# Kernel optimization log

Hardware: AMD Instinct MI355X
Metric: run time of the kernel (lower is better)

The kernel has to match this reference:

```python
import jax, jax.numpy as jnp
import numpy as np

NUM_K = 10
T = 1.0  # softmax temperature (forward default)


def setup_inputs() -> dict:
    key = jax.random.key(0)
    k1, k2, k3, k4 = jax.random.split(key, 4)
    B, H, P, D = 64, 12, 197, 64
    return {
        "att_s": jax.random.normal(k1, (B, H, P, P), dtype=jnp.float32),
        "att_t": jax.random.normal(k2, (B, H, P, P), dtype=jnp.float32),
        "v_s": jax.random.normal(k3, (B, H, P, D), dtype=jnp.float32),
        "v_t": jax.random.normal(k4, (B, H, P, D), dtype=jnp.float32),
    }


def _topk_masked_attend(att, v):
    # att: [B,H,P,P] logits, v: [B,H,P,D]
    a = jax.nn.softmax(att / T, axis=-1)
    # kth-largest value per row acts as the threshold (torch.topk semantics)
    margin = jax.lax.top_k(a, NUM_K)[0][..., -1]           # [B,H,P]
    a = a * (a >= margin[..., None])                        # keep top-k entries
    norm = a.sum(-1)                                        # [B,H,P]
    return jnp.einsum("bhpq,bhqd->bhpd", a, v) / norm[..., None]


def reference(att_s, att_t, v_s, v_t):
    out_s = _topk_masked_attend(att_s, v_s)
    out_t = _topk_masked_attend(att_t, v_t)
    # nn.MSELoss default reduction='mean'
    return jnp.mean(jnp.square(out_s - out_t))
```

## Files before the change

### kernel.cpp

```cpp
#include <hip/hip_runtime.h>
#include <cstdint>
#include <cfloat>

#define NK 10
constexpr int Pp   = 197;
constexpr int Dd   = 64;
constexpr int ROWS = 64 * 12 * 197;
constexpr int BLK  = 256;
constexpr int RPB  = 256;
constexpr int NBLK = ROWS / RPB;
constexpr int CH   = 32;
constexpr int NFULL = Pp / CH;
constexpr int TAIL  = Pp - NFULL * CH;
constexpr float INV_N = 1.0f / 9682944.0f;

constexpr int RPB_B = 16;
constexpr int NB_B  = ROWS / RPB_B;

__device__ __forceinline__ uint32_t fbits(float x) { return __float_as_uint(x); }
__device__ __forceinline__ float    bfl(uint32_t u) { return __uint_as_float(u); }

template <int CW>
__device__ __forceinline__ void consume_chunk(const float* __restrict__ trow,
                                              float a[NK]) {
#pragma unroll
  for (int j = 0; j < CW; ++j) {
    float x = trow[j];
#pragma unroll
    for (int s = 0; s < NK - 1; ++s) a[s] = fmaxf(a[s], fminf(x, a[s + 1]));
    a[NK - 1] = fmaxf(a[NK - 1], x);
  }
}

__device__ __forceinline__ void load_chunk_regs(const float* __restrict__ slab,
                                                int c, int t, float pf[CH]) {
  if (c < NFULL) {
    const int r0 = t >> 5, j = t & 31;
    const uint32_t col = (uint32_t)(c * CH + j);
    const float* p = slab + c * CH + r0 * Pp + j;
#pragma unroll
    for (int i = 0; i < CH; ++i) {
      float x = __builtin_nontemporal_load(&p[i * 8 * Pp]);
      pf[i] = bfl((fbits(x) & 0xFFFFFF00u) | col);
    }
  } else {
    const float* cbase = slab + NFULL * CH;
#pragma unroll
    for (int i = 0; i < TAIL; ++i) {
      int e = t + i * BLK;
      int r = e / TAIL, j = e % TAIL;
      float x = __builtin_nontemporal_load(&cbase[r * Pp + j]);
      pf[i] = bfl((fbits(x) & 0xFFFFFF00u) | (uint32_t)(NFULL * CH + j));
    }
  }
}

__device__ __forceinline__ void store_chunk(float (*tile)[CH + 1], int c, int t,
                                            const float pf[CH]) {
  if (c < NFULL) {
    const int r0 = t >> 5, j = t & 31;
#pragma unroll
    for (int i = 0; i < CH; ++i) tile[r0 + 8 * i][j] = pf[i];
  } else {
#pragma unroll
    for (int i = 0; i < TAIL; ++i) {
      int e = t + i * BLK;
      tile[e / TAIL][e % TAIL] = pf[i];
    }
  }
}

__global__ __launch_bounds__(BLK, 4) void select_kernel(
    const float* __restrict__ att_s, const float* __restrict__ att_t,
    float* __restrict__ wpk ) {
  __shared__ float tile[RPB][CH + 1];

  const int t = threadIdx.x;
  const int bi = blockIdx.x;
  const int tensor = (bi >= NBLK) ? 1 : 0;
  const int slab = bi - tensor * NBLK;
  const float* A = tensor ? att_t : att_s;
  const int blockRow0 = slab * RPB;

  float a[NK];
#pragma unroll
  for (int k = 0; k < NK; ++k) a[k] = -FLT_MAX;

  const float* slabp = A + (size_t)blockRow0 * Pp;
  float pf[CH];

  load_chunk_regs(slabp, 0, t, pf);
  for (int c = 0; c <= NFULL; ++c) {
    __syncthreads();
    store_chunk(tile, c, t, pf);
    __syncthreads();
    if (c < NFULL) {
      load_chunk_regs(slabp, c + 1, t, pf);
      consume_chunk<CH>(tile[t], a);
    } else {
      consume_chunk<TAIL>(tile[t], a);
    }
  }

  float mx = a[NK - 1];
  float e[NK], s = 0.f;
#pragma unroll
  for (int k = 0; k < NK; ++k) { e[k] = __expf(a[k] - mx); s += e[k]; }
  float inv = 1.0f / s;

  __syncthreads();
  float* flat = &tile[0][0];
#pragma unroll
  for (int k = 0; k < NK; ++k) {
    float w = e[k] * inv;
    flat[t * NK + k] = bfl((fbits(w) & 0xFFFFFF00u) | (fbits(a[k]) & 0xFFu));
  }
  __syncthreads();
  float* dst = wpk + ((size_t)tensor * ROWS + blockRow0) * NK;
#pragma unroll
  for (int i = 0; i < NK; ++i) dst[t + i * BLK] = flat[t + i * BLK];
}

__global__ __launch_bounds__(1024) void gather_kernel(
    const float* __restrict__ v_s, const float* __restrict__ v_t,
    const float* __restrict__ wpk, float* __restrict__ partial) {
  const int t = threadIdx.x, wv = t >> 6, l = t & 63;
  int row = blockIdx.x * RPB_B + wv;
  row = __builtin_amdgcn_readfirstlane(row);
  const int bh = row / Pp;
  const float* vsb = v_s + (size_t)bh * (Pp * Dd) + l;
  const float* vtb = v_t + (size_t)bh * (Pp * Dd) + l;
  const float* w0 = wpk + (size_t)row * NK;
  const float* w1 = wpk + ((size_t)ROWS + row) * NK;

  float acc = 0.f;
#pragma unroll
  for (int k = 0; k < NK; ++k) {
    float w = w0[k];
    int idx = (int)(fbits(w) & 0xFFu);
    acc = fmaf(w, vsb[idx * Dd], acc);
  }
#pragma unroll
  for (int k = 0; k < NK; ++k) {
    float w = w1[k];
    int idx = (int)(fbits(w) & 0xFFu);
    acc = fmaf(-w, vtb[idx * Dd], acc);
  }
  float sq = acc * acc;
#pragma unroll
  for (int off = 32; off > 0; off >>= 1) sq += __shfl_xor(sq, off, 64);

  __shared__ float red[RPB_B];
  if (l == 0) red[wv] = sq;
  __syncthreads();
  if (t == 0) {
    float tot = 0.f;
#pragma unroll
    for (int i = 0; i < RPB_B; ++i) tot += red[i];
    partial[blockIdx.x] = tot;
  }
}

__global__ __launch_bounds__(1024) void reduce_kernel(
    const float* __restrict__ partial, float* __restrict__ out) {
  const int t = threadIdx.x, wv = t >> 6, l = t & 63;
  float s = 0.f;
  for (int i = t; i < NB_B; i += 1024) s += partial[i];
#pragma unroll
  for (int off = 32; off > 0; off >>= 1) s += __shfl_xor(s, off, 64);
  __shared__ float red[16];
  if (l == 0) red[wv] = s;
  __syncthreads();
  if (t == 0) {
    float tot = 0.f;
#pragma unroll
    for (int i = 0; i < 16; ++i) tot += red[i];
    out[0] = tot * INV_N;
  }
}

extern "C" void kernel_launch(void* const* d_in, const int* in_sizes, int n_in,
                              void* d_out, int out_size, void* d_ws,
                              size_t ws_size, hipStream_t stream) {
  const float* att_s = (const float*)d_in[0];
  const float* att_t = (const float*)d_in[1];
  const float* v_s = (const float*)d_in[2];
  const float* v_t = (const float*)d_in[3];
  float* out = (float*)d_out;

  float* wpk = (float*)d_ws;
  float* partial = wpk + (size_t)2 * ROWS * NK;

  select_kernel<<<2 * NBLK, BLK, 0, stream>>>(att_s, att_t, wpk);
  gather_kernel<<<NB_B, 1024, 0, stream>>>(v_s, v_t, wpk, partial);
  reduce_kernel<<<1, 1024, 0, stream>>>(partial, out);
}
```

Before: 379.0 us.

## Split each row's top-k across two threads with pairwise insertion and vector loads

The select kernel now assigns two threads per row, each keeping a top-10 over half the columns, and merges them with a bitonic-style max of one list against the other's reversed top half via lane shuffles. Global loads become 16-byte vector loads, the tile stride is padded for vector LDS access, and elements are inserted two at a time with a pair-insert network. Rows per block drop to 128 and the occupancy hint rises to 8, aiming for more parallelism and fewer instructions per element in this compute-bound selection step. The merge keeps only the top 5 of the elementwise maxes, which is valid for a bitonic merge, and unaligned f4 loads depend on the declared 4-byte alignment.

```diff
diff --git a/kernel.cpp b/kernel.cpp
--- a/kernel.cpp
+++ b/kernel.cpp
@@ -7,118 +7,152 @@
 constexpr int Dd   = 64;
 constexpr int ROWS = 64 * 12 * 197;
 constexpr int BLK  = 256;
-constexpr int RPB  = 256;
-constexpr int NBLK = ROWS / RPB;
+constexpr int RPB  = 128;
+constexpr int NSLAB = ROWS / RPB;
 constexpr int CH   = 32;
-constexpr int NFULL = Pp / CH;
-constexpr int TAIL  = Pp - NFULL * CH;
+constexpr int NCH  = Pp / CH;
+constexpr int TAILC = Pp - NCH * CH;
+constexpr int LDW  = CH + 4;
 constexpr float INV_N = 1.0f / 9682944.0f;
 
 constexpr int RPB_B = 16;
 constexpr int NB_B  = ROWS / RPB_B;
 
+typedef float f4 __attribute__((ext_vector_type(4), aligned(4)));
+
 __device__ __forceinline__ uint32_t fbits(float x) { return __float_as_uint(x); }
 __device__ __forceinline__ float    bfl(uint32_t u) { return __uint_as_float(u); }
 
-template <int CW>
-__device__ __forceinline__ void consume_chunk(const float* __restrict__ trow,
-                                              float a[NK]) {
-#pragma unroll
-  for (int j = 0; j < CW; ++j) {
-    float x = trow[j];
-#pragma unroll
-    for (int s = 0; s < NK - 1; ++s) a[s] = fmaxf(a[s], fminf(x, a[s + 1]));
-    a[NK - 1] = fmaxf(a[NK - 1], x);
-  }
-}
-
-__device__ __forceinline__ void load_chunk_regs(const float* __restrict__ slab,
-                                                int c, int t, float pf[CH]) {
-  if (c < NFULL) {
-    const int r0 = t >> 5, j = t & 31;
-    const uint32_t col = (uint32_t)(c * CH + j);
-    const float* p = slab + c * CH + r0 * Pp + j;
-#pragma unroll
-    for (int i = 0; i < CH; ++i) {
-      float x = __builtin_nontemporal_load(&p[i * 8 * Pp]);
-      pf[i] = bfl((fbits(x) & 0xFFFFFF00u) | col);
+__device__ __forceinline__ void pair_insert(float a[NK], float x0, float x1) {
+  float u = fminf(x0, x1), v = fmaxf(x0, x1);
+#pragma unroll
+  for (int s = 0; s < 8; ++s) {
+    float t1 = fminf(a[s + 1], v), t2 = fminf(a[s + 2], u);
+    a[s] = fmaxf(fmaxf(a[s], t1), t2);
+  }
+  float t1 = fminf(a[9], v);
+  a[8] = fmaxf(fmaxf(a[8], t1), u);
+  a[9] = fmaxf(a[9], v);
+}
+
+__device__ __forceinline__ void one_insert(float a[NK], float x) {
+#pragma unroll
+  for (int s = 0; s < 9; ++s) a[s] = fmaxf(a[s], fminf(x, a[s + 1]));
+  a[9] = fmaxf(a[9], x);
+}
+
+__device__ __forceinline__ void load_chunk(const float* __restrict__ sp, int c,
+                                           int t, f4 pf[4]) {
+#pragma unroll
+  for (int i = 0; i < 4; ++i) {
+    int f = t + BLK * i;
+    int rr = f >> 3, c4 = f & 7;
+    const f4* p = (const f4*)(sp + rr * Pp + c * CH + c4 * 4);
+    f4 q = __builtin_nontemporal_load(p);
+    uint32_t cb = (uint32_t)(c * CH + c4 * 4);
+    q.x = bfl((fbits(q.x) & 0xFFFFFF00u) | cb);
+    q.y = bfl((fbits(q.y) & 0xFFFFFF00u) | (cb + 1));
+    q.z = bfl((fbits(q.z) & 0xFFFFFF00u) | (cb + 2));
+    q.w = bfl((fbits(q.w) & 0xFFFFFF00u) | (cb + 3));
+    pf[i] = q;
+  }
+}
+
+__device__ __forceinline__ void load_tail(const float* __restrict__ sp, int t,
+                                          float tpf[3]) {
+#pragma unroll
+  for (int i = 0; i < 3; ++i) {
+    int e = t + BLK * i;
+    if (e < RPB * TAILC) {
+      int rr = e / TAILC, j = e % TAILC;
+      float x = __builtin_nontemporal_load(sp + rr * Pp + NCH * CH + j);
+      tpf[i] = bfl((fbits(x) & 0xFFFFFF00u) | (uint32_t)(NCH * CH + j));
     }
-  } else {
-    const float* cbase = slab + NFULL * CH;
-#pragma unroll
-    for (int i = 0; i < TAIL; ++i) {
-      int e = t + i * BLK;
-      int r = e / TAIL, j = e % TAIL;
-      float x = __builtin_nontemporal_load(&cbase[r * Pp + j]);
-      pf[i] = bfl((fbits(x) & 0xFFFFFF00u) | (uint32_t)(NFULL * CH + j));
-    }
-  }
-}
-
-__device__ __forceinline__ void store_chunk(float (*tile)[CH + 1], int c, int t,
-                                            const float pf[CH]) {
-  if (c < NFULL) {
-    const int r0 = t >> 5, j = t & 31;
-#pragma unroll
-    for (int i = 0; i < CH; ++i) tile[r0 + 8 * i][j] = pf[i];
-  } else {
-#pragma unroll
-    for (int i = 0; i < TAIL; ++i) {
-      int e = t + i * BLK;
-      tile[e / TAIL][e % TAIL] = pf[i];
-    }
-  }
-}
-
-__global__ __launch_bounds__(BLK, 4) void select_kernel(
+  }
+}
+
+__global__ __launch_bounds__(BLK, 8) void select_kernel(
     const float* __restrict__ att_s, const float* __restrict__ att_t,
     float* __restrict__ wpk ) {
-  __shared__ float tile[RPB][CH + 1];
+  __shared__ float tile[RPB][LDW];
 
   const int t = threadIdx.x;
   const int bi = blockIdx.x;
-  const int tensor = (bi >= NBLK) ? 1 : 0;
-  const int slab = bi - tensor * NBLK;
+  const int tensor = (bi >= NSLAB) ? 1 : 0;
+  const int slab = bi - tensor * NSLAB;
   const float* A = tensor ? att_t : att_s;
-  const int blockRow0 = slab * RPB;
+  const int row0 = slab * RPB;
+  const float* sp = A + (size_t)row0 * Pp;
+  const int r = t >> 1, h = t & 1;
 
   float a[NK];
 #pragma unroll
   for (int k = 0; k < NK; ++k) a[k] = -FLT_MAX;
 
-  const float* slabp = A + (size_t)blockRow0 * Pp;
-  float pf[CH];
-
-  load_chunk_regs(slabp, 0, t, pf);
-  for (int c = 0; c <= NFULL; ++c) {
+  f4 pf[4];
+  float tpf[3];
+  load_chunk(sp, 0, t, pf);
+
+  for (int c = 0; c < NCH; ++c) {
     __syncthreads();
-    store_chunk(tile, c, t, pf);
+#pragma unroll
+    for (int i = 0; i < 4; ++i) {
+      int f = t + BLK * i;
+      *((f4*)&tile[f >> 3][(f & 7) * 4]) = pf[i];
+    }
     __syncthreads();
-    if (c < NFULL) {
-      load_chunk_regs(slabp, c + 1, t, pf);
-      consume_chunk<CH>(tile[t], a);
-    } else {
-      consume_chunk<TAIL>(tile[t], a);
+    if (c + 1 < NCH) load_chunk(sp, c + 1, t, pf);
+    else load_tail(sp, t, tpf);
+#pragma unroll
+    for (int j4 = 0; j4 < 4; ++j4) {
+      f4 q = *((const f4*)&tile[r][16 * h + 4 * j4]);
+      pair_insert(a, q.x, q.y);
+      pair_insert(a, q.z, q.w);
     }
   }
-
-  float mx = a[NK - 1];
-  float e[NK], s = 0.f;
-#pragma unroll
-  for (int k = 0; k < NK; ++k) { e[k] = __expf(a[k] - mx); s += e[k]; }
-  float inv = 1.0f / s;
-
-  __syncthreads();
+  __syncthreads();
+#pragma unroll
+  for (int i = 0; i < 3; ++i) {
+    int e = t + BLK * i;
+    if (e < RPB * TAILC) tile[e / TAILC][e % TAILC] = tpf[i];
+  }
+  __syncthreads();
+  if (h == 0) {
+    pair_insert(a, tile[r][0], tile[r][1]);
+    one_insert(a, tile[r][4]);
+  } else {
+    pair_insert(a, tile[r][2], tile[r][3]);
+  }
+
+  float b5 = __shfl_xor(a[5], 1, 64), b6 = __shfl_xor(a[6], 1, 64);
+  float b7 = __shfl_xor(a[7], 1, 64), b8 = __shfl_xor(a[8], 1, 64);
+  float b9 = __shfl_xor(a[9], 1, 64);
+  float m[5];
+  m[0] = fmaxf(a[0], b9);
+  m[1] = fmaxf(a[1], b8);
+  m[2] = fmaxf(a[2], b7);
+  m[3] = fmaxf(a[3], b6);
+  m[4] = fmaxf(a[4], b5);
+  float mx = fmaxf(a[9], b9);
+
+  float ev[5], s5 = 0.f;
+#pragma unroll
+  for (int i = 0; i < 5; ++i) { ev[i] = __expf(m[i] - mx); s5 += ev[i]; }
+  float stot = s5 + __shfl_xor(s5, 1, 64);
+  float inv = 1.0f / stot;
+
   float* flat = &tile[0][0];
-#pragma unroll
-  for (int k = 0; k < NK; ++k) {
-    float w = e[k] * inv;
-    flat[t * NK + k] = bfl((fbits(w) & 0xFFFFFF00u) | (fbits(a[k]) & 0xFFu));
-  }
-  __syncthreads();
-  float* dst = wpk + ((size_t)tensor * ROWS + blockRow0) * NK;
-#pragma unroll
-  for (int i = 0; i < NK; ++i) dst[t + i * BLK] = flat[t + i * BLK];
+  __syncthreads();
+#pragma unroll
+  for (int i = 0; i < 5; ++i) {
+    float w = ev[i] * inv;
+    flat[r * NK + 5 * h + i] =
+        bfl((fbits(w) & 0xFFFFFF00u) | (fbits(m[i]) & 0xFFu));
+  }
+  __syncthreads();
+  float* dst = wpk + ((size_t)tensor * ROWS + row0) * NK;
+#pragma unroll
+  for (int i = 0; i < 5; ++i) dst[t + BLK * i] = flat[t + BLK * i];
 }
 
 __global__ __launch_bounds__(1024) void gather_kernel(
@@ -191,7 +225,7 @@
   float* wpk = (float*)d_ws;
   float* partial = wpk + (size_t)2 * ROWS * NK;
 
-  select_kernel<<<2 * NBLK, BLK, 0, stream>>>(att_s, att_t, wpk);
+  select_kernel<<<2 * NSLAB, BLK, 0, stream>>>(att_s, att_t, wpk);
   gather_kernel<<<NB_B, 1024, 0, stream>>>(v_s, v_t, wpk, partial);
   reduce_kernel<<<1, 1024, 0, stream>>>(partial, out);
 }
```

New measurement: 391.3 us. 3.2% more time.
